# Performance work log

Measured on AMD Instinct MI355X. Metric: run time of the kernel, lower is better.

The kernel has to match this reference:

```python
import jax, jax.numpy as jnp
import numpy as np

B, T, F, H, D = 64, 256, 128, 8, 256
E = F * H          # MHA embed dim = input_dim * feat_dim = 1024
HEADS = 4
HD = E // HEADS


def setup_inputs() -> dict:
    key = jax.random.key(0)
    ks = jax.random.split(key, 12)
    def w(k, shape, fan_in):
        return (jax.random.normal(k, shape, jnp.float32) / np.float32(np.sqrt(fan_in)))
    z = lambda *s: jnp.zeros(s, jnp.float32)
    return {
        "x": jax.random.normal(ks[0], (B, T, F), jnp.float32),
        # input_attn MLP: Linear(F, F//4) -> GELU -> Linear(F//4, F) -> Sigmoid
        "attn_w1": w(ks[1], (F, F // 4), F), "attn_b1": z(F // 4),
        "attn_w2": w(ks[2], (F // 4, F), F // 4), "attn_b2": z(F),
        # bank of F tiny GRUs (input=1, hidden=H), stacked along feature axis
        "W_ih": w(ks[3], (F, 3 * H), 1),        # input weight per feature (input size 1)
        "W_hh": w(ks[4], (F, 3 * H, H), H),
        "b_ih": z(F, 3 * H), "b_hh": z(F, 3 * H),
        # MultiheadAttention(E, 4 heads)
        "in_proj_w": w(ks[5], (E, 3 * E), E), "in_proj_b": z(3 * E),
        "mha_out_w": w(ks[6], (E, E), E), "mha_out_b": z(E),
        # out_proj: Linear(E, D)
        "outp_w": w(ks[7], (E, D), E), "outp_b": z(D),
        # FFN: Linear(D, 2D) -> GELU -> Linear(2D, D)
        "ffn_w1": w(ks[8], (D, 2 * D), D), "ffn_b1": z(2 * D),
        "ffn_w2": w(ks[9], (2 * D, D), 2 * D), "ffn_b2": z(D),
    }


def _forward(x, attn_w1, attn_b1, attn_w2, attn_b2,
             W_ih, W_hh, b_ih, b_hh,
             in_proj_w, in_proj_b, mha_out_w, mha_out_b,
             outp_w, outp_b, ffn_w1, ffn_b1, ffn_w2, ffn_b2):
    gelu = lambda v: jax.nn.gelu(v, approximate=False)
    bs, ts, _ = x.shape
    # feature gating (dropout layers are identity in eval mode)
    input_attn = jax.nn.sigmoid(gelu(x @ attn_w1 + attn_b1) @ attn_w2 + attn_b2)  # [B,T,F]
    xg = x * input_attn

    # fused bank of F independent GRUs (input size 1, hidden H), scanned over time
    def step(h, xt):  # h: [B,F,H], xt: [B,F]
        gi = xt[..., None] * W_ih + b_ih                       # [B,F,3H]
        gh = jnp.einsum('bfh,fgh->bfg', h, W_hh) + b_hh        # [B,F,3H]
        ir, iz, inn = jnp.split(gi, 3, axis=-1)
        hr, hz, hn = jnp.split(gh, 3, axis=-1)
        r = jax.nn.sigmoid(ir + hr)
        zg = jax.nn.sigmoid(iz + hz)
        n = jnp.tanh(inn + r * hn)
        h_new = (1.0 - zg) * n + zg * h
        return h_new, h_new

    h0 = jnp.zeros((bs, F, H), x.dtype)
    _, ys = jax.lax.scan(step, h0, jnp.moveaxis(xg, 1, 0))     # ys: [T,B,F,H]
    out = jnp.moveaxis(ys, 0, 1).reshape(bs, ts, E)            # [B,T,E]

    # self-attention (eval: no dropout)
    qkv = out @ in_proj_w + in_proj_b                          # [B,T,3E]
    q, k, v = jnp.split(qkv, 3, axis=-1)
    hsplit = lambda t: t.reshape(bs, ts, HEADS, HD)
    q, k, v = hsplit(q), hsplit(k), hsplit(v)
    scores = jnp.einsum('bqhd,bkhd->bhqk', q, k) / np.float32(np.sqrt(HD))
    attn = jax.nn.softmax(scores, axis=-1)
    ctx = jnp.einsum('bhqk,bkhd->bqhd', attn, v).reshape(bs, ts, E)
    mha_out = ctx @ mha_out_w + mha_out_b

    h1 = mha_out @ outp_w + outp_b                             # [B,T,D]
    ffn = gelu(h1 @ ffn_w1 + ffn_b1) @ ffn_w2 + ffn_b2
    y = h1 + ffn
    feature_importance = input_attn.sum(-1)                    # [B,T]
    return y, feature_importance, input_attn


def reference(x, attn_w1, attn_b1, attn_w2, attn_b2,
              W_ih, W_hh, b_ih, b_hh,
              in_proj_w, in_proj_b, mha_out_w, mha_out_b,
              outp_w, outp_b, ffn_w1, ffn_b1, ffn_w2, ffn_b2):
    return _forward(x, attn_w1, attn_b1, attn_w2, attn_b2,
                    W_ih, W_hh, b_ih, b_hh,
                    in_proj_w, in_proj_b, mha_out_w, mha_out_b,
                    outp_w, outp_b, ffn_w1, ffn_b1, ffn_w2, ffn_b2)
```

## Files before the change

kernel.cpp:

```cpp
#include <hip/hip_runtime.h>
#include <hip/hip_bf16.h>
#include <math.h>

#define B_  64
#define T_  256
#define F_  128
#define H_  8
#define E_  1024
#define NH_ 4
#define HD_ 256
#define D_  256

#define OFF_Y_  0L
#define OFF_FI_ 4194304L
#define OFF_IA_ 4210688L

typedef unsigned short u16;
typedef unsigned int   u32;
typedef short bf16x8 __attribute__((ext_vector_type(8)));
typedef float f32x4  __attribute__((ext_vector_type(4)));

__device__ __forceinline__ float bf2f(u16 u) {
  union { u32 u; float f; } x; x.u = ((u32)u) << 16; return x.f;
}
__device__ __forceinline__ u16 f2bf(float f) {
  union { float f; u32 u; } x; x.f = f;
  u32 r = (x.u + 0x7fffu + ((x.u >> 16) & 1u)) >> 16;
  return (u16)r;
}
__device__ __forceinline__ float gelu_exact(float v) {
  return 0.5f * v * (1.f + erff(v * 0.70710678118654752f));
}
__device__ __forceinline__ float sigmoidf_(float v) {
  return 1.f / (1.f + __expf(-v));
}
__device__ __forceinline__ float ldv(const void* p, long i, bool isf) {
  return isf ? ((const float*)p)[i] : bf2f(((const u16*)p)[i]);
}
__device__ __forceinline__ void stv(void* p, long i, float v, bool isf) {
  if (isf) ((float*)p)[i] = v;
  else ((u16*)p)[i] = f2bf(v);
}
__device__ __forceinline__ void gld16(void* lds, const void* g) {
  __builtin_amdgcn_global_load_lds(
      (const __attribute__((address_space(1))) u32*)g,
      (__attribute__((address_space(3))) u32*)lds, 16, 0, 0);
}

__global__ void detect_dtype(const u16* __restrict__ x, u32* __restrict__ flag) {
  if (threadIdx.x == 0 && blockIdx.x == 0) {
    int good = 0;
    for (int i = 0; i < 512; ++i) {
      u16 v = x[i];
      int e = (v >> 7) & 0xFF;
      if (v == 0 || (e >= 100 && e <= 140)) ++good;
    }
    *flag = (good >= 450) ? 0u : 1u;
  }
}

__global__ __launch_bounds__(256)
void convert_in(const void* __restrict__ src, u16* __restrict__ dst, int n,
                const u32* __restrict__ flag) {
  const bool isf = (*flag != 0);
  int i = blockIdx.x * 256 + threadIdx.x;
  if (i < n) dst[i] = isf ? f2bf(((const float*)src)[i]) : ((const u16*)src)[i];
}

__global__ void transpose_cvt(const void* __restrict__ in, u16* __restrict__ out,
                              int R, int C, const u32* __restrict__ flag) {
  const bool isf = (*flag != 0);
  __shared__ float t[32][33];
  const int c0 = blockIdx.x * 32, r0 = blockIdx.y * 32;
  const int tx = threadIdx.x, ty = threadIdx.y;
  for (int i = ty; i < 32; i += 8)
    t[i][tx] = ldv(in, (long)(r0 + i) * C + c0 + tx, isf);
  __syncthreads();
  for (int i = ty; i < 32; i += 8)
    out[(long)(c0 + i) * R + r0 + tx] = f2bf(t[tx][i]);
}

__global__ __launch_bounds__(128)
void input_mlp2(const void* __restrict__ x,
                const void* __restrict__ w1, const void* __restrict__ b1,
                const void* __restrict__ w2, const void* __restrict__ b2,
                const u32* __restrict__ flag,
                u16* __restrict__ xg, void* __restrict__ dout) {
  const bool isf = (*flag != 0);
  const long row = blockIdx.x;
  const int tid = threadIdx.x;
  __shared__ float xr[F_];
  __shared__ float hid4[4][32];
  __shared__ float hid[32];
  __shared__ float red[2];
  float xv = ldv(x, row * F_ + tid, isf);
  xr[tid] = xv;
  __syncthreads();
  {
    const int g = tid & 31, part = tid >> 5;
    const int f0 = part * 32;
    float s = 0.f;
    #pragma unroll 8
    for (int f = 0; f < 32; ++f) s += xr[f0 + f] * ldv(w1, (long)(f0 + f) * 32 + g, isf);
    hid4[part][g] = s;
  }
  __syncthreads();
  if (tid < 32)
    hid[tid] = gelu_exact(ldv(b1, tid, isf) + hid4[0][tid] + hid4[1][tid]
                          + hid4[2][tid] + hid4[3][tid]);
  __syncthreads();
  float s = ldv(b2, tid, isf);
  #pragma unroll 8
  for (int j = 0; j < 32; ++j) s += hid[j] * ldv(w2, j * F_ + tid, isf);
  float ia = sigmoidf_(s);
  stv(dout, OFF_IA_ + row * F_ + tid, ia, isf);
  xg[row * F_ + tid] = f2bf(ia * xv);
  float v = ia;
  for (int o = 32; o > 0; o >>= 1) v += __shfl_down(v, o);
  if ((tid & 63) == 0) red[tid >> 6] = v;
  __syncthreads();
  if (tid == 0) stv(dout, OFF_FI_ + row, red[0] + red[1], isf);
}

__global__ __launch_bounds__(256)
void gru_scan4(const u16* __restrict__ xg, const void* __restrict__ W_ih,
               const void* __restrict__ W_hh, const void* __restrict__ b_ih,
               const void* __restrict__ b_hh, const u32* __restrict__ flag,
               u16* __restrict__ gruo) {
  const bool isf = (*flag != 0);
  const int tid = threadIdx.x;
  const int ric = tid >> 3;
  const int j   = tid & 7;
  const int rec = blockIdx.x * 32 + ric;
  const int b = rec >> 7, f = rec & 127;
  __shared__ __align__(16) float hbuf[32][8];
  float whr[8], whz[8], whn[8];
  #pragma unroll
  for (int k = 0; k < 8; ++k) {
    whr[k] = ldv(W_hh, (long)f * 192 + j * 8 + k, isf);
    whz[k] = ldv(W_hh, (long)f * 192 + (8 + j) * 8 + k, isf);
    whn[k] = ldv(W_hh, (long)f * 192 + (16 + j) * 8 + k, isf);
  }
  const float wir = ldv(W_ih, f * 24 + j, isf);
  const float wiz = ldv(W_ih, f * 24 + 8 + j, isf);
  const float win = ldv(W_ih, f * 24 + 16 + j, isf);
  const float cbr = ldv(b_ih, f * 24 + j, isf) + ldv(b_hh, f * 24 + j, isf);
  const float cbz = ldv(b_ih, f * 24 + 8 + j, isf) + ldv(b_hh, f * 24 + 8 + j, isf);
  const float bin_ = ldv(b_ih, f * 24 + 16 + j, isf);
  const float bhn_ = ldv(b_hh, f * 24 + 16 + j, isf);
  float h[8];
  #pragma unroll
  for (int k = 0; k < 8; ++k) h[k] = 0.f;
  const u16* xp = xg + (long)b * T_ * F_ + f;
  u16* op = gruo + (long)b * T_ * E_ + f * 8 + j;
  float xv = bf2f(xp[0]);
  for (int t = 0; t < T_; ++t) {
    float xn = (t + 1 < T_) ? bf2f(xp[(t + 1) * F_]) : 0.f;
    float ar = fmaf(xv, wir, cbr);
    float az = fmaf(xv, wiz, cbz);
    float an = bhn_;
    #pragma unroll
    for (int k = 0; k < 8; ++k) {
      ar = fmaf(h[k], whr[k], ar);
      az = fmaf(h[k], whz[k], az);
      an = fmaf(h[k], whn[k], an);
    }
    const float r = sigmoidf_(ar);
    const float z = sigmoidf_(az);
    const float a = fmaf(r, an, fmaf(xv, win, bin_));
    const float e = __expf(2.f * a);
    const float n = 1.f - 2.f / (e + 1.f);
    const float hn = fmaf(z, h[j] - n, n);
    op[(long)t * E_] = f2bf(hn);
    hbuf[ric][j] = hn;
    f32x4 h0 = *(const f32x4*)&hbuf[ric][0];
    f32x4 h1 = *(const f32x4*)&hbuf[ric][4];
    h[0] = h0[0]; h[1] = h0[1]; h[2] = h0[2]; h[3] = h0[3];
    h[4] = h1[0]; h[5] = h1[1]; h[6] = h1[2]; h[7] = h1[3];
    xv = xn;
  }
}

template <int EPI>
__global__ __launch_bounds__(256)
void gemm_bt(const u16* __restrict__ A, int lda,
             const u16* __restrict__ Bp, int ldb,
             u16* __restrict__ Cg, int ldc,
             const u16* __restrict__ bias,
             int K, int nbm) {
  const int bm = blockIdx.x % nbm, bn = blockIdx.x / nbm;
  const int w = threadIdx.x >> 6, lane = threadIdx.x & 63;
  __shared__ __align__(16) u16 As[128 * 64];
  __shared__ __align__(16) u16 Bs[128 * 64];
  const long m0 = (long)bm * 128, n0 = (long)bn * 128;
  const int wm = w >> 1, wn = w & 1;
  const int lr8 = lane >> 3;
  const int csw = ((lane & 7) ^ (lr8 & 7)) * 8;
  f32x4 acc[4][4] = {};
  const int nk = K >> 6;
  const int lr = lane & 15, lq = lane >> 4;
  for (int kt = 0; kt < nk; ++kt) {
    const int k0 = kt << 6;
    __syncthreads();
    #pragma unroll
    for (int c = 0; c < 4; ++c) {
      const int rb = w * 32 + c * 8;
      gld16((char*)As + rb * 128, A + (m0 + rb + lr8) * (long)lda + k0 + csw);
      gld16((char*)Bs + rb * 128, Bp + (n0 + rb + lr8) * (long)ldb + k0 + csw);
    }
    __syncthreads();
    #pragma unroll
    for (int sub = 0; sub < 2; ++sub) {
      const int ch = sub * 4 + lq;
      const int cof = ((ch ^ (lr & 7)) << 3);
      bf16x8 af[4], bfv[4];
      #pragma unroll
      for (int i = 0; i < 4; ++i)
        af[i] = *(const bf16x8*)&As[(wm * 64 + i * 16 + lr) * 64 + cof];
      #pragma unroll
      for (int i = 0; i < 4; ++i)
        bfv[i] = *(const bf16x8*)&Bs[(wn * 64 + i * 16 + lr) * 64 + cof];
      #pragma unroll
      for (int i = 0; i < 4; ++i) {
        #pragma unroll
        for (int j = 0; j < 4; ++j)
          acc[i][j] = __builtin_amdgcn_mfma_f32_16x16x32_bf16(af[i], bfv[j], acc[i][j], 0, 0, 0);
      }
    }
  }
  const int rq = lq * 4;
  #pragma unroll
  for (int j = 0; j < 4; ++j) {
    const long col = n0 + wn * 64 + j * 16 + lr;
    const float bv = (EPI >= 1) ? bf2f(bias[col]) : 0.f;
    #pragma unroll
    for (int i = 0; i < 4; ++i) {
      const long row0 = m0 + wm * 64 + i * 16 + rq;
      #pragma unroll
      for (int q = 0; q < 4; ++q)
        Cg[(row0 + q) * (long)ldc + col] = f2bf(acc[i][j][q] + bv);
    }
  }
}

__global__ __launch_bounds__(256)
void fused_tail(const u16* __restrict__ MHA,
                const u16* __restrict__ wtO, const u16* __restrict__ wtF1,
                const u16* __restrict__ wtF2,
                const u16* __restrict__ bO, const u16* __restrict__ bF1,
                const u16* __restrict__ bF2,
                void* __restrict__ Y, const u32* __restrict__ flag) {
  const bool isf = (*flag != 0);
  const int w = threadIdx.x >> 6, lane = threadIdx.x & 63;
  const long m0 = (long)blockIdx.x * 32;
  __shared__ __align__(16) u16 Astg[32 * 64];
  __shared__ __align__(16) u16 h1s[32 * 264];
  __shared__ __align__(16) u16 ffhs[32 * 520];
  const int lr = lane & 15, lq = lane >> 4;
  const int rq = lq * 4;
  const int srow = w * 8 + (lane >> 3);
  const int csw = ((lane & 7) ^ ((lane >> 3) & 7)) * 8;
  f32x4 acc1[2][4] = {};
  for (int kt = 0; kt < 16; ++kt) {
    const int k0 = kt << 6;
    __syncthreads();
    gld16(&Astg[w * 512], MHA + (m0 + srow) * 1024L + k0 + csw);
    __syncthreads();
    #pragma unroll
    for (int kk = 0; kk < 2; ++kk) {
      const int ch = kk * 4 + lq;
      const int cof = ((ch ^ (lr & 7)) << 3);
      bf16x8 af[2];
      #pragma unroll
      for (int i = 0; i < 2; ++i)
        af[i] = *(const bf16x8*)&Astg[(i * 16 + lr) * 64 + cof];
      #pragma unroll
      for (int j = 0; j < 4; ++j) {
        const int n = w * 64 + j * 16 + lr;
        bf16x8 bfv = *(const bf16x8*)(wtO + n * 1024L + k0 + kk * 32 + lq * 8);
        #pragma unroll
        for (int i = 0; i < 2; ++i)
          acc1[i][j] = __builtin_amdgcn_mfma_f32_16x16x32_bf16(af[i], bfv, acc1[i][j], 0, 0, 0);
      }
    }
  }
  __syncthreads();
  #pragma unroll
  for (int j = 0; j < 4; ++j) {
    const int col = w * 64 + j * 16 + lr;
    const float bv = bf2f(bO[col]);
    #pragma unroll
    for (int i = 0; i < 2; ++i)
      #pragma unroll
      for (int q = 0; q < 4; ++q)
        h1s[(i * 16 + rq + q) * 264 + col] = f2bf(acc1[i][j][q] + bv);
  }
  __syncthreads();
  f32x4 acc2[2][8] = {};
  for (int kt = 0; kt < 8; ++kt) {
    const int k0 = kt << 5;
    bf16x8 af[2];
    #pragma unroll
    for (int i = 0; i < 2; ++i)
      af[i] = *(const bf16x8*)&h1s[(i * 16 + lr) * 264 + k0 + lq * 8];
    #pragma unroll
    for (int j = 0; j < 8; ++j) {
      const int n = w * 128 + j * 16 + lr;
      bf16x8 bfv = *(const bf16x8*)(wtF1 + n * 256L + k0 + lq * 8);
      #pragma unroll
      for (int i = 0; i < 2; ++i)
        acc2[i][j] = __builtin_amdgcn_mfma_f32_16x16x32_bf16(af[i], bfv, acc2[i][j], 0, 0, 0);
    }
  }
  __syncthreads();
  #pragma unroll
  for (int j = 0; j < 8; ++j) {
    const int col = w * 128 + j * 16 + lr;
    const float bv = bf2f(bF1[col]);
    #pragma unroll
    for (int i = 0; i < 2; ++i)
      #pragma unroll
      for (int q = 0; q < 4; ++q)
        ffhs[(i * 16 + rq + q) * 520 + col] = f2bf(gelu_exact(acc2[i][j][q] + bv));
  }
  __syncthreads();
  f32x4 acc3[2][4] = {};
  for (int kt = 0; kt < 16; ++kt) {
    const int k0 = kt << 5;
    bf16x8 af[2];
    #pragma unroll
    for (int i = 0; i < 2; ++i)
      af[i] = *(const bf16x8*)&ffhs[(i * 16 + lr) * 520 + k0 + lq * 8];
    #pragma unroll
    for (int j = 0; j < 4; ++j) {
      const int n = w * 64 + j * 16 + lr;
      bf16x8 bfv = *(const bf16x8*)(wtF2 + n * 512L + k0 + lq * 8);
      #pragma unroll
      for (int i = 0; i < 2; ++i)
        acc3[i][j] = __builtin_amdgcn_mfma_f32_16x16x32_bf16(af[i], bfv, acc3[i][j], 0, 0, 0);
    }
  }
  #pragma unroll
  for (int j = 0; j < 4; ++j) {
    const int col = w * 64 + j * 16 + lr;
    const float bv = bf2f(bF2[col]);
    #pragma unroll
    for (int i = 0; i < 2; ++i)
      #pragma unroll
      for (int q = 0; q < 4; ++q) {
        const int rl = i * 16 + rq + q;
        const float v = acc3[i][j][q] + bv + bf2f(h1s[rl * 264 + col]);
        stv(Y, (m0 + rl) * 256L + col, v, isf);
      }
  }
}

__global__ __launch_bounds__(256)
void attn_fused(const u16* __restrict__ qkv, u16* __restrict__ ctx) {
  const int z = blockIdx.y, bb = z >> 2, hh = z & 3;
  const int w = threadIdx.x >> 6, lane = threadIdx.x & 63;
  const int tid = threadIdx.x;
  const long t0 = (long)blockIdx.x * 64;
  __shared__ __align__(16) u16 P1[10240];
  __shared__ __align__(16) u16 Pl[64 * 264];
  __shared__ __align__(16) u16 Vt[256 * 40];
  const u16* qb = qkv + (long)bb * T_ * 3 * E_ + hh * HD_;
  const u16* kb = qb + E_;
  const u16* vb = qb + 2 * E_;
  const int rr = lane >> 2, cc = lane & 3;
  const int lr = lane & 15, lq = lane >> 4, lk = lq * 8;
  f32x4 acc[16] = {};
  for (int kt = 0; kt < 8; ++kt) {
    const int k0 = kt * 32;
    __syncthreads();
    gld16((char*)P1 + w * 16 * 64, qb + (t0 + w * 16 + rr) * (3L * E_) + k0 + cc * 8);
    #pragma unroll
    for (int c = 0; c < 4; ++c) {
      const int rb = w * 64 + c * 16;
      gld16((char*)P1 + 4096 + rb * 64, kb + (long)(rb + rr) * (3L * E_) + k0 + cc * 8);
    }
    __syncthreads();
    bf16x8 aq = *(const bf16x8*)&P1[(w * 16 + lr) * 32 + lk];
    #pragma unroll
    for (int nt = 0; nt < 16; ++nt) {
      bf16x8 bk = *(const bf16x8*)&P1[2048 + (nt * 16 + lr) * 32 + lk];
      acc[nt] = __builtin_amdgcn_mfma_f32_16x16x32_bf16(aq, bk, acc[nt], 0, 0, 0);
    }
  }
  #pragma unroll
  for (int q = 0; q < 4; ++q) {
    float mx = -3.4e38f;
    #pragma unroll
    for (int nt = 0; nt < 16; ++nt) mx = fmaxf(mx, acc[nt][q]);
    mx = fmaxf(mx, __shfl_xor(mx, 1));
    mx = fmaxf(mx, __shfl_xor(mx, 2));
    mx = fmaxf(mx, __shfl_xor(mx, 4));
    mx = fmaxf(mx, __shfl_xor(mx, 8));
    float e[16], sum = 0.f;
    #pragma unroll
    for (int nt = 0; nt < 16; ++nt) {
      e[nt] = __expf((acc[nt][q] - mx) * 0.0625f);
      sum += e[nt];
    }
    sum += __shfl_xor(sum, 1);
    sum += __shfl_xor(sum, 2);
    sum += __shfl_xor(sum, 4);
    sum += __shfl_xor(sum, 8);
    const float inv = 1.f / sum;
    const int rowl = w * 16 + lq * 4 + q;
    #pragma unroll
    for (int nt = 0; nt < 16; ++nt)
      Pl[rowl * 264 + nt * 16 + lr] = f2bf(e[nt] * inv);
  }
  f32x4 acc2[16] = {};
  for (int st = 0; st < 8; ++st) {
    const int s0 = st * 32;
    __syncthreads();
    #pragma unroll
    for (int c = 0; c < 4; ++c) {
      const int rb = w * 8 + c * 2;
      gld16((char*)P1 + rb * 512, vb + (s0 + rb + (lane >> 5)) * (3L * E_) + (lane & 31) * 8);
    }
    __syncthreads();
    u16 col[32];
    #pragma unroll
    for (int si = 0; si < 32; ++si) col[si] = P1[si * 256 + tid];
    #pragma unroll
    for (int cq = 0; cq < 4; ++cq)
      *(uint4*)&Vt[tid * 40 + cq * 8] = *(const uint4*)&col[cq * 8];
    __syncthreads();
    bf16x8 pa = *(const bf16x8*)&Pl[(w * 16 + lr) * 264 + s0 + lk];
    #pragma unroll
    for (int nt = 0; nt < 16; ++nt) {
      bf16x8 bv = *(const bf16x8*)&Vt[(nt * 16 + lr) * 40 + lk];
      acc2[nt] = __builtin_amdgcn_mfma_f32_16x16x32_bf16(pa, bv, acc2[nt], 0, 0, 0);
    }
  }
  const int rq = lq * 4;
  #pragma unroll
  for (int nt = 0; nt < 16; ++nt) {
    const int cold = nt * 16 + lr;
    #pragma unroll
    for (int q = 0; q < 4; ++q) {
      const long row = t0 + w * 16 + rq + q;
      ctx[((long)bb * T_ + row) * E_ + hh * HD_ + cold] = f2bf(acc2[nt][q]);
    }
  }
}

extern "C" void kernel_launch(void* const* d_in, const int* in_sizes, int n_in,
                              void* d_out, int out_size, void* d_ws, size_t ws_size,
                              hipStream_t stream) {
  (void)in_sizes; (void)n_in; (void)out_size; (void)ws_size;
  char* ws = (char*)d_ws;
  u16* BIASA = (u16*)(ws + 0);
  u32* FLAG  = (u32*)(ws + 12288);
  u16* wtI   = (u16*)(ws + 65536);
  u16* wtM   = (u16*)(ws + 6356992);
  u16* wtO   = (u16*)(ws + 8454144);
  u16* wtF1  = (u16*)(ws + 8978432);
  u16* wtF2  = (u16*)(ws + 9240576);
  u16* XG    = (u16*)(ws + 9502720);
  u16* GRUO  = (u16*)(ws + 16777216);
  u16* CTX   = GRUO;
  u16* QKV   = (u16*)(ws + 50331648);
  u16* MHA   = (u16*)(ws + 50331648);

  detect_dtype<<<1, 64, 0, stream>>>((const u16*)d_in[0], FLAG);

  convert_in<<<12, 256, 0, stream>>>(d_in[10], BIASA + 0,    3072, FLAG);
  convert_in<<<4,  256, 0, stream>>>(d_in[12], BIASA + 3072, 1024, FLAG);
  convert_in<<<1,  256, 0, stream>>>(d_in[14], BIASA + 4096, 256,  FLAG);
  convert_in<<<2,  256, 0, stream>>>(d_in[16], BIASA + 4352, 512,  FLAG);
  convert_in<<<1,  256, 0, stream>>>(d_in[18], BIASA + 4864, 256,  FLAG);

  dim3 tb(32, 8);
  transpose_cvt<<<dim3(3072 / 32, 1024 / 32), tb, 0, stream>>>(d_in[9],  wtI,  1024, 3072, FLAG);
  transpose_cvt<<<dim3(1024 / 32, 1024 / 32), tb, 0, stream>>>(d_in[11], wtM,  1024, 1024, FLAG);
  transpose_cvt<<<dim3(256 / 32, 1024 / 32),  tb, 0, stream>>>(d_in[13], wtO,  1024, 256,  FLAG);
  transpose_cvt<<<dim3(512 / 32, 256 / 32),   tb, 0, stream>>>(d_in[15], wtF1, 256,  512,  FLAG);
  transpose_cvt<<<dim3(256 / 32, 512 / 32),   tb, 0, stream>>>(d_in[17], wtF2, 512,  256,  FLAG);

  input_mlp2<<<B_ * T_, 128, 0, stream>>>(d_in[0], d_in[1], d_in[2], d_in[3], d_in[4],
                                          FLAG, XG, d_out);
  gru_scan4<<<256, 256, 0, stream>>>(XG, d_in[5], d_in[6], d_in[7], d_in[8], FLAG, GRUO);

  gemm_bt<1><<<dim3(128 * 24, 1), 256, 0, stream>>>(GRUO, 1024, wtI, 1024,
      QKV, 3072, BIASA, 1024, 128);
  attn_fused<<<dim3(4, B_ * NH_), 256, 0, stream>>>(QKV, CTX);
  gemm_bt<1><<<dim3(128 * 8, 1), 256, 0, stream>>>(CTX, 1024, wtM, 1024,
      MHA, 1024, BIASA + 3072, 1024, 128);
  fused_tail<<<512, 256, 0, stream>>>(MHA, wtO, wtF1, wtF2,
      BIASA + 4096, BIASA + 4352, BIASA + 4864, d_out, FLAG);
}
```

Baseline: 447.9 us.

## Fuse MHA output projection into the tail kernel and merge bias conversions

Removes the separate MHA out-projection GEMM and the old fused_tail, replacing them with one mega_tail kernel. Each block handles 64 rows: it computes ctx@W_mha in 256-column chunks held in LDS and accumulates each chunk straight into the out_proj GEMM, then runs the FFN. This avoids writing and re-reading the 1024-wide MHA intermediate through global memory. The five bias conversion launches also become a single kernel. In exchange, only 256 blocks of 4 waves run with about 140KB of LDS each, W_mha and W_out are read from global memory without LDS staging in every block, and the ctx tile is reloaded for each of the four column chunks. That may cost occupancy and add cache traffic.

```diff
diff --git a/kernel.cpp b/kernel.cpp
--- a/kernel.cpp
+++ b/kernel.cpp
@@ -46,6 +46,7 @@
       (const __attribute__((address_space(1))) u32*)g,
       (__attribute__((address_space(3))) u32*)lds, 16, 0, 0);
 }
+#define MFMA_ __builtin_amdgcn_mfma_f32_16x16x32_bf16
 
 __global__ void detect_dtype(const u16* __restrict__ x, u32* __restrict__ flag) {
   if (threadIdx.x == 0 && blockIdx.x == 0) {
@@ -60,11 +61,19 @@
 }
 
 __global__ __launch_bounds__(256)
-void convert_in(const void* __restrict__ src, u16* __restrict__ dst, int n,
-                const u32* __restrict__ flag) {
+void convert_biases(const void* __restrict__ s0, const void* __restrict__ s1,
+                    const void* __restrict__ s2, const void* __restrict__ s3,
+                    const void* __restrict__ s4,
+                    u16* __restrict__ dst, const u32* __restrict__ flag) {
   const bool isf = (*flag != 0);
-  int i = blockIdx.x * 256 + threadIdx.x;
-  if (i < n) dst[i] = isf ? f2bf(((const float*)src)[i]) : ((const u16*)src)[i];
+  const int i = blockIdx.x * 256 + threadIdx.x;
+  const void* s; long off;
+  if (i < 3072)      { s = s0; off = i; }
+  else if (i < 4096) { s = s1; off = i - 3072; }
+  else if (i < 4352) { s = s2; off = i - 4096; }
+  else if (i < 4864) { s = s3; off = i - 4352; }
+  else               { s = s4; off = i - 4864; }
+  if (i < 5120) dst[i] = f2bf(ldv(s, off, isf));
 }
 
 __global__ void transpose_cvt(const void* __restrict__ in, u16* __restrict__ out,
@@ -224,7 +233,7 @@
       for (int i = 0; i < 4; ++i) {
         #pragma unroll
         for (int j = 0; j < 4; ++j)
-          acc[i][j] = __builtin_amdgcn_mfma_f32_16x16x32_bf16(af[i], bfv[j], acc[i][j], 0, 0, 0);
+          acc[i][j] = MFMA_(af[i], bfv[j], acc[i][j], 0, 0, 0);
       }
     }
   }
@@ -240,118 +249,6 @@
       for (int q = 0; q < 4; ++q)
         Cg[(row0 + q) * (long)ldc + col] = f2bf(acc[i][j][q] + bv);
     }
-  }
-}
-
-__global__ __launch_bounds__(256)
-void fused_tail(const u16* __restrict__ MHA,
-                const u16* __restrict__ wtO, const u16* __restrict__ wtF1,
-                const u16* __restrict__ wtF2,
-                const u16* __restrict__ bO, const u16* __restrict__ bF1,
-                const u16* __restrict__ bF2,
-                void* __restrict__ Y, const u32* __restrict__ flag) {
-  const bool isf = (*flag != 0);
-  const int w = threadIdx.x >> 6, lane = threadIdx.x & 63;
-  const long m0 = (long)blockIdx.x * 32;
-  __shared__ __align__(16) u16 Astg[32 * 64];
-  __shared__ __align__(16) u16 h1s[32 * 264];
-  __shared__ __align__(16) u16 ffhs[32 * 520];
-  const int lr = lane & 15, lq = lane >> 4;
-  const int rq = lq * 4;
-  const int srow = w * 8 + (lane >> 3);
-  const int csw = ((lane & 7) ^ ((lane >> 3) & 7)) * 8;
-  f32x4 acc1[2][4] = {};
-  for (int kt = 0; kt < 16; ++kt) {
-    const int k0 = kt << 6;
-    __syncthreads();
-    gld16(&Astg[w * 512], MHA + (m0 + srow) * 1024L + k0 + csw);
-    __syncthreads();
-    #pragma unroll
-    for (int kk = 0; kk < 2; ++kk) {
-      const int ch = kk * 4 + lq;
-      const int cof = ((ch ^ (lr & 7)) << 3);
-      bf16x8 af[2];
-      #pragma unroll
-      for (int i = 0; i < 2; ++i)
-        af[i] = *(const bf16x8*)&Astg[(i * 16 + lr) * 64 + cof];
-      #pragma unroll
-      for (int j = 0; j < 4; ++j) {
-        const int n = w * 64 + j * 16 + lr;
-        bf16x8 bfv = *(const bf16x8*)(wtO + n * 1024L + k0 + kk * 32 + lq * 8);
-        #pragma unroll
-        for (int i = 0; i < 2; ++i)
-          acc1[i][j] = __builtin_amdgcn_mfma_f32_16x16x32_bf16(af[i], bfv, acc1[i][j], 0, 0, 0);
-      }
-    }
-  }
-  __syncthreads();
-  #pragma unroll
-  for (int j = 0; j < 4; ++j) {
-    const int col = w * 64 + j * 16 + lr;
-    const float bv = bf2f(bO[col]);
-    #pragma unroll
-    for (int i = 0; i < 2; ++i)
-      #pragma unroll
-      for (int q = 0; q < 4; ++q)
-        h1s[(i * 16 + rq + q) * 264 + col] = f2bf(acc1[i][j][q] + bv);
-  }
-  __syncthreads();
-  f32x4 acc2[2][8] = {};
-  for (int kt = 0; kt < 8; ++kt) {
-    const int k0 = kt << 5;
-    bf16x8 af[2];
-    #pragma unroll
-    for (int i = 0; i < 2; ++i)
-      af[i] = *(const bf16x8*)&h1s[(i * 16 + lr) * 264 + k0 + lq * 8];
-    #pragma unroll
-    for (int j = 0; j < 8; ++j) {
-      const int n = w * 128 + j * 16 + lr;
-      bf16x8 bfv = *(const bf16x8*)(wtF1 + n * 256L + k0 + lq * 8);
-      #pragma unroll
-      for (int i = 0; i < 2; ++i)
-        acc2[i][j] = __builtin_amdgcn_mfma_f32_16x16x32_bf16(af[i], bfv, acc2[i][j], 0, 0, 0);
-    }
-  }
-  __syncthreads();
-  #pragma unroll
-  for (int j = 0; j < 8; ++j) {
-    const int col = w * 128 + j * 16 + lr;
-    const float bv = bf2f(bF1[col]);
-    #pragma unroll
-    for (int i = 0; i < 2; ++i)
-      #pragma unroll
-      for (int q = 0; q < 4; ++q)
-        ffhs[(i * 16 + rq + q) * 520 + col] = f2bf(gelu_exact(acc2[i][j][q] + bv));
-  }
-  __syncthreads();
-  f32x4 acc3[2][4] = {};
-  for (int kt = 0; kt < 16; ++kt) {
-    const int k0 = kt << 5;
-    bf16x8 af[2];
-    #pragma unroll
-    for (int i = 0; i < 2; ++i)
-      af[i] = *(const bf16x8*)&ffhs[(i * 16 + lr) * 520 + k0 + lq * 8];
-    #pragma unroll
-    for (int j = 0; j < 4; ++j) {
-      const int n = w * 64 + j * 16 + lr;
-      bf16x8 bfv = *(const bf16x8*)(wtF2 + n * 512L + k0 + lq * 8);
-      #pragma unroll
-      for (int i = 0; i < 2; ++i)
-        acc3[i][j] = __builtin_amdgcn_mfma_f32_16x16x32_bf16(af[i], bfv, acc3[i][j], 0, 0, 0);
-    }
-  }
-  #pragma unroll
-  for (int j = 0; j < 4; ++j) {
-    const int col = w * 64 + j * 16 + lr;
-    const float bv = bf2f(bF2[col]);
-    #pragma unroll
-    for (int i = 0; i < 2; ++i)
-      #pragma unroll
-      for (int q = 0; q < 4; ++q) {
-        const int rl = i * 16 + rq + q;
-        const float v = acc3[i][j][q] + bv + bf2f(h1s[rl * 264 + col]);
-        stv(Y, (m0 + rl) * 256L + col, v, isf);
-      }
   }
 }
 
@@ -384,7 +281,7 @@
     #pragma unroll
     for (int nt = 0; nt < 16; ++nt) {
       bf16x8 bk = *(const bf16x8*)&P1[2048 + (nt * 16 + lr) * 32 + lk];
-      acc[nt] = __builtin_amdgcn_mfma_f32_16x16x32_bf16(aq, bk, acc[nt], 0, 0, 0);
+      acc[nt] = MFMA_(aq, bk, acc[nt], 0, 0, 0);
     }
   }
   #pragma unroll
@@ -433,7 +330,7 @@
     #pragma unroll
     for (int nt = 0; nt < 16; ++nt) {
       bf16x8 bv = *(const bf16x8*)&Vt[(nt * 16 + lr) * 40 + lk];
-      acc2[nt] = __builtin_amdgcn_mfma_f32_16x16x32_bf16(pa, bv, acc2[nt], 0, 0, 0);
+      acc2[nt] = MFMA_(pa, bv, acc2[nt], 0, 0, 0);
     }
   }
   const int rq = lq * 4;
@@ -445,6 +342,148 @@
       const long row = t0 + w * 16 + rq + q;
       ctx[((long)bb * T_ + row) * E_ + hh * HD_ + cold] = f2bf(acc2[nt][q]);
     }
+  }
+}
+
+__global__ __launch_bounds__(256)
+void mega_tail(const u16* __restrict__ ctxp,
+               const u16* __restrict__ wtM, const u16* __restrict__ wtO,
+               const u16* __restrict__ wtF1, const u16* __restrict__ wtF2,
+               const u16* __restrict__ bM, const u16* __restrict__ bO,
+               const u16* __restrict__ bF1, const u16* __restrict__ bF2,
+               void* __restrict__ Y, const u32* __restrict__ flag) {
+  const bool isf = (*flag != 0);
+  const int w = threadIdx.x >> 6, lane = threadIdx.x & 63;
+  const long m0 = (long)blockIdx.x * 64;
+  __shared__ __align__(16) u16 As[64 * 64];
+  __shared__ __align__(16) u16 Mcs[64 * 264];
+  __shared__ __align__(16) u16 h1s[64 * 264];
+  __shared__ __align__(16) u16 ffhs[64 * 520];
+  const int lr = lane & 15, lq = lane >> 4;
+  const int lr8 = lane >> 3;
+  const int csw = ((lane & 7) ^ (lr8 & 7)) * 8;
+  f32x4 acc1[4][4] = {};
+  for (int cc = 0; cc < 4; ++cc) {
+    f32x4 acc0[4][4] = {};
+    for (int kt = 0; kt < 16; ++kt) {
+      const int k0 = kt << 6;
+      __syncthreads();
+      #pragma unroll
+      for (int c = 0; c < 2; ++c) {
+        const int rb = w * 16 + c * 8;
+        gld16((char*)As + rb * 128, ctxp + (m0 + rb + lr8) * 1024L + k0 + csw);
+      }
+      __syncthreads();
+      #pragma unroll
+      for (int kk = 0; kk < 2; ++kk) {
+        const int ch = kk * 4 + lq;
+        const int cof = ((ch ^ (lr & 7)) << 3);
+        bf16x8 af[4];
+        #pragma unroll
+        for (int i = 0; i < 4; ++i)
+          af[i] = *(const bf16x8*)&As[(i * 16 + lr) * 64 + cof];
+        #pragma unroll
+        for (int j = 0; j < 4; ++j) {
+          const int n = cc * 256 + w * 64 + j * 16 + lr;
+          bf16x8 bfv = *(const bf16x8*)(wtM + (long)n * 1024 + k0 + kk * 32 + lq * 8);
+          #pragma unroll
+          for (int i = 0; i < 4; ++i)
+            acc0[i][j] = MFMA_(af[i], bfv, acc0[i][j], 0, 0, 0);
+        }
+      }
+    }
+    #pragma unroll
+    for (int j = 0; j < 4; ++j) {
+      const int coll = w * 64 + j * 16 + lr;
+      const float bv = bf2f(bM[cc * 256 + coll]);
+      #pragma unroll
+      for (int i = 0; i < 4; ++i)
+        #pragma unroll
+        for (int q = 0; q < 4; ++q)
+          Mcs[(i * 16 + lq * 4 + q) * 264 + coll] = f2bf(acc0[i][j][q] + bv);
+    }
+    __syncthreads();
+    for (int ks = 0; ks < 8; ++ks) {
+      bf16x8 af[4];
+      #pragma unroll
+      for (int i = 0; i < 4; ++i)
+        af[i] = *(const bf16x8*)&Mcs[(i * 16 + lr) * 264 + ks * 32 + lq * 8];
+      #pragma unroll
+      for (int j = 0; j < 4; ++j) {
+        const int n = w * 64 + j * 16 + lr;
+        bf16x8 bfv = *(const bf16x8*)(wtO + (long)n * 1024 + cc * 256 + ks * 32 + lq * 8);
+        #pragma unroll
+        for (int i = 0; i < 4; ++i)
+          acc1[i][j] = MFMA_(af[i], bfv, acc1[i][j], 0, 0, 0);
+      }
+    }
+  }
+  #pragma unroll
+  for (int j = 0; j < 4; ++j) {
+    const int coll = w * 64 + j * 16 + lr;
+    const float bv = bf2f(bO[coll]);
+    #pragma unroll
+    for (int i = 0; i < 4; ++i)
+      #pragma unroll
+      for (int q = 0; q < 4; ++q)
+        h1s[(i * 16 + lq * 4 + q) * 264 + coll] = f2bf(acc1[i][j][q] + bv);
+  }
+  __syncthreads();
+  {
+    f32x4 acc2[4][8] = {};
+    for (int ks = 0; ks < 8; ++ks) {
+      bf16x8 af[4];
+      #pragma unroll
+      for (int i = 0; i < 4; ++i)
+        af[i] = *(const bf16x8*)&h1s[(i * 16 + lr) * 264 + ks * 32 + lq * 8];
+      #pragma unroll
+      for (int j = 0; j < 8; ++j) {
+        const int n = w * 128 + j * 16 + lr;
+        bf16x8 bfv = *(const bf16x8*)(wtF1 + (long)n * 256 + ks * 32 + lq * 8);
+        #pragma unroll
+        for (int i = 0; i < 4; ++i)
+          acc2[i][j] = MFMA_(af[i], bfv, acc2[i][j], 0, 0, 0);
+      }
+    }
+    #pragma unroll
+    for (int j = 0; j < 8; ++j) {
+      const int coll = w * 128 + j * 16 + lr;
+      const float bv = bf2f(bF1[coll]);
+      #pragma unroll
+      for (int i = 0; i < 4; ++i)
+        #pragma unroll
+        for (int q = 0; q < 4; ++q)
+          ffhs[(i * 16 + lq * 4 + q) * 520 + coll] = f2bf(gelu_exact(acc2[i][j][q] + bv));
+    }
+  }
+  __syncthreads();
+  f32x4 acc3[4][4] = {};
+  for (int ks = 0; ks < 16; ++ks) {
+    bf16x8 af[4];
+    #pragma unroll
+    for (int i = 0; i < 4; ++i)
+      af[i] = *(const bf16x8*)&ffhs[(i * 16 + lr) * 520 + ks * 32 + lq * 8];
+    #pragma unroll
+    for (int j = 0; j < 4; ++j) {
+      const int n = w * 64 + j * 16 + lr;
+      bf16x8 bfv = *(const bf16x8*)(wtF2 + (long)n * 512 + ks * 32 + lq * 8);
+      #pragma unroll
+      for (int i = 0; i < 4; ++i)
+        acc3[i][j] = MFMA_(af[i], bfv, acc3[i][j], 0, 0, 0);
+    }
+  }
+  #pragma unroll
+  for (int j = 0; j < 4; ++j) {
+    const int coll = w * 64 + j * 16 + lr;
+    const float bv = bf2f(bF2[coll]);
+    #pragma unroll
+    for (int i = 0; i < 4; ++i)
+      #pragma unroll
+      for (int q = 0; q < 4; ++q) {
+        const int rowl = i * 16 + lq * 4 + q;
+        const float v = acc3[i][j][q] + bv + bf2f(h1s[rowl * 264 + coll]);
+        stv(Y, (m0 + rowl) * 256L + coll, v, isf);
+      }
   }
 }
 
@@ -464,15 +503,10 @@
   u16* GRUO  = (u16*)(ws + 16777216);
   u16* CTX   = GRUO;
   u16* QKV   = (u16*)(ws + 50331648);
-  u16* MHA   = (u16*)(ws + 50331648);
 
   detect_dtype<<<1, 64, 0, stream>>>((const u16*)d_in[0], FLAG);
-
-  convert_in<<<12, 256, 0, stream>>>(d_in[10], BIASA + 0,    3072, FLAG);
-  convert_in<<<4,  256, 0, stream>>>(d_in[12], BIASA + 3072, 1024, FLAG);
-  convert_in<<<1,  256, 0, stream>>>(d_in[14], BIASA + 4096, 256,  FLAG);
-  convert_in<<<2,  256, 0, stream>>>(d_in[16], BIASA + 4352, 512,  FLAG);
-  convert_in<<<1,  256, 0, stream>>>(d_in[18], BIASA + 4864, 256,  FLAG);
+  convert_biases<<<20, 256, 0, stream>>>(d_in[10], d_in[12], d_in[14], d_in[16],
+                                         d_in[18], BIASA, FLAG);
 
   dim3 tb(32, 8);
   transpose_cvt<<<dim3(3072 / 32, 1024 / 32), tb, 0, stream>>>(d_in[9],  wtI,  1024, 3072, FLAG);
@@ -488,8 +522,7 @@
   gemm_bt<1><<<dim3(128 * 24, 1), 256, 0, stream>>>(GRUO, 1024, wtI, 1024,
       QKV, 3072, BIASA, 1024, 128);
   attn_fused<<<dim3(4, B_ * NH_), 256, 0, stream>>>(QKV, CTX);
-  gemm_bt<1><<<dim3(128 * 8, 1), 256, 0, stream>>>(CTX, 1024, wtM, 1024,
-      MHA, 1024, BIASA + 3072, 1024, 128);
-  fused_tail<<<512, 256, 0, stream>>>(MHA, wtO, wtF1, wtF2,
-      BIASA + 4096, BIASA + 4352, BIASA + 4864, d_out, FLAG);
-}
+  mega_tail<<<256, 256, 0, stream>>>(CTX, wtM, wtO, wtF1, wtF2,
+      BIASA + 3072, BIASA + 4096, BIASA + 4352, BIASA + 4864,
+      d_out, FLAG);
+}
```

Measured after the change: 586.2 us. 1.31x slower.
